# Kernel optimization log

Measured on AMD Instinct MI355X. Metric: run time of the kernel, lower is better.

Reference implementation:

```python
import jax, jax.numpy as jnp
import numpy as np
from jax import lax

K = 5          # CARAFE kernel_size
S = 2          # scale_factor (downsample stride)
GROUP = 1      # mask groups
ENC_PAD = 1    # (encoder_kernel-1)*dilation//2 with encoder_kernel=3


def _conv2d(x, w, b, stride, padding, dilation=1):
    y = lax.conv_general_dilated(
        x, w, window_strides=(stride, stride),
        padding=[(padding, padding), (padding, padding)],
        rhs_dilation=(dilation, dilation),
        dimension_numbers=('NCHW', 'OIHW', 'NCHW'))
    return y + b[None, :, None, None]


def setup_inputs() -> dict:
    key = jax.random.key(0)
    k1, k2, k3 = jax.random.split(key, 3)
    B, C, H, W = 4, 256, 128, 128
    COMP = 64
    x = jax.random.normal(k1, (B, C, H, W), dtype=jnp.float32)
    # xavier-uniform-ish scale for compressor, std=0.001 for content encoder (as in init_weights)
    w1 = jax.random.normal(k2, (COMP, C, 1, 1), dtype=jnp.float32) * (1.0 / np.sqrt(C))
    b1 = jnp.zeros((COMP,), dtype=jnp.float32)
    w2 = jax.random.normal(k3, (K * K * GROUP, COMP, 3, 3), dtype=jnp.float32) * 0.001
    b2 = jnp.zeros((K * K * GROUP,), dtype=jnp.float32)
    return {"x": x, "w1": w1, "b1": b1, "w2": w2, "b2": b2}


def _carafe_forward(x, w1, b1, w2, b2):
    B, C, H, W = x.shape
    compressed = _conv2d(x, w1, b1, stride=1, padding=0)           # (B, 64, H, W)
    mask = _conv2d(compressed, w2, b2, stride=S, padding=ENC_PAD)   # (B, K*K*G, Ho, Wo)
    Ho, Wo = mask.shape[2], mask.shape[3]
    # kernel_normalizer: softmax over the K*K window per group
    mask = jax.nn.softmax(mask.reshape(B, GROUP, K * K, Ho, Wo), axis=2)
    # feature_reassemble: fused unfold * mask sum — accumulate per kernel tap to
    # avoid materializing the full (B, C, K*K, Ho, Wo) tensor.
    pad = K // 2
    x_pad = jnp.pad(x, ((0, 0), (0, 0), (pad, pad), (pad, pad)))
    Cg = C // GROUP
    out = jnp.zeros((B, GROUP, Cg, Ho, Wo), dtype=x.dtype)
    for i in range(K):
        for j in range(K):
            patch = x_pad[:, :, i:i + S * (Ho - 1) + 1:S, j:j + S * (Wo - 1) + 1:S]
            patch = patch.reshape(B, GROUP, Cg, Ho, Wo)
            out = out + patch * mask[:, :, i * K + j][:, :, None]
    return out.reshape(B, C, Ho, Wo)


def reference(x, w1, b1, w2, b2):
    return _carafe_forward(x, w1, b1, w2, b2)
```

## Files before the change

### kernel.cpp

```cpp
#include <hip/hip_runtime.h>
#include <math.h>

#define BN   4
#define CN   256
#define HN   128
#define WN   128
#define COMP 64
#define KK   25
#define HO   64
#define WO   64

#define TB_OFF    36864
#define SM_OFF    37120
#define SM_SLICE  (BN * HO * KK * 64)
#define XT_OFF    (SM_OFF + SM_SLICE)
#define WS_NEED   ((size_t)(XT_OFF + (size_t)BN * HN * WN * CN / 2) * 4)

typedef short v8s  __attribute__((ext_vector_type(8)));
typedef float v16f __attribute__((ext_vector_type(16)));

__device__ inline ushort f2bf(float f) {
  unsigned u = __float_as_uint(f);
  return (ushort)((u + 0x7fffu + ((u >> 16) & 1u)) >> 16);
}

__global__ __launch_bounds__(256) void prep_kernel(
    const float* __restrict__ x, const float* __restrict__ w1,
    const float* __restrict__ b1, const float* __restrict__ w2,
    float* __restrict__ ws) {
  const int bid = blockIdx.x;
  const int tid = threadIdx.x;
  if (bid < 4096) {
    __shared__ float st[64][65];
    const int b = bid >> 10, h = (bid >> 3) & 127, bx = bid & 7;
    const int wt = bx & 1, ct = bx >> 1;
    const int w0 = wt * 64, c0 = ct * 64;
    {
      const int wl = tid & 63, cw = tid >> 6;
#pragma unroll
      for (int i = 0; i < 16; ++i) {
        int cl = cw * 16 + i;
        st[cl][wl] = x[((size_t)(b * CN + c0 + cl) * HN + h) * WN + w0 + wl];
      }
    }
    __syncthreads();
    ushort* xT = (ushort*)(ws + XT_OFF);
    const int cg = tid & 15, wl0 = tid >> 4;
#pragma unroll
    for (int wi = 0; wi < 4; ++wi) {
      int wl = wl0 + wi * 16;
      ushort4 o = make_ushort4(f2bf(st[cg * 4 + 0][wl]), f2bf(st[cg * 4 + 1][wl]),
                               f2bf(st[cg * 4 + 2][wl]), f2bf(st[cg * 4 + 3][wl]));
      *(ushort4*)(xT + ((size_t)((b * HN + h) * WN + w0 + wl)) * CN + c0 + cg * 4) = o;
    }
  } else {
    const int cid = bid - 4096;
    const int t = cid >> 2;
    const int chunk = (cid & 3) * 4 + (tid >> 6);
    const int lane = tid & 63;
    const int m = lane & 31, half = lane >> 5;
    const int c0 = chunk * 16 + half * 8;
    float acc[8] = {0.f, 0.f, 0.f, 0.f, 0.f, 0.f, 0.f, 0.f};
    if (m < KK) {
      for (int k = 0; k < COMP; ++k) {
        float wv = w2[(size_t)(m * COMP + k) * 9 + t];
        const float* w1r = w1 + (size_t)k * CN + c0;
        float4 a = *(const float4*)w1r;
        float4 bq = *(const float4*)(w1r + 4);
        acc[0] += wv * a.x;  acc[1] += wv * a.y;
        acc[2] += wv * a.z;  acc[3] += wv * a.w;
        acc[4] += wv * bq.x; acc[5] += wv * bq.y;
        acc[6] += wv * bq.z; acc[7] += wv * bq.w;
      }
    }
    ushort* wA = (ushort*)ws;
    ushort pk[8];
#pragma unroll
    for (int j = 0; j < 8; ++j) pk[j] = f2bf(acc[j]);
    *(ushort4*)(wA + ((size_t)(t * 16 + chunk) * 64 + lane) * 8) =
        make_ushort4(pk[0], pk[1], pk[2], pk[3]);
    *(ushort4*)(wA + ((size_t)(t * 16 + chunk) * 64 + lane) * 8 + 4) =
        make_ushort4(pk[4], pk[5], pk[6], pk[7]);
    if (chunk == 0 && lane < KK) {
      float tbv = 0.f;
      for (int k = 0; k < COMP; ++k)
        tbv += w2[(size_t)(lane * COMP + k) * 9 + t] * b1[k];
      ws[TB_OFF + lane * 9 + t] = tbv;
    }
  }
}

__global__ __launch_bounds__(512) void conv_softmax(
    const float* __restrict__ ws, const float* __restrict__ b2,
    float* __restrict__ sm) {
  const int ho = blockIdx.x, b = blockIdx.y;
  const int tid = threadIdx.x;
  const int lane = tid & 63;
  const int z = tid >> 6;
  const int n = lane & 31, half = lane >> 5;
  const ushort* xT = (const ushort*)(ws + XT_OFF);
  const ushort* wA = (const ushort*)ws;
  const int coff = z * 32 + half * 8;
  const v8s zero8 = {};
  v16f acc[2] = {{}, {}};

  __shared__ float red[8 * KK * 64];

#pragma unroll
  for (int dr = 0; dr < 3; ++dr) {
    const int r = 2 * ho + dr - 1;
    if (r < 0) continue;
#pragma unroll
    for (int dc = 0; dc < 3; ++dc) {
      const int t = dr * 3 + dc;
      const ushort* ap = wA + ((size_t)(t * 16 + z * 2) * 64 + lane) * 8;
      v8s af0 = *(const v8s*)ap;
      v8s af1 = *(const v8s*)(ap + 512);
      const size_t rowbase = (size_t)((b * HN + r) * WN);
#pragma unroll
      for (int wt = 0; wt < 2; ++wt) {
        const int wo = wt * 32 + n;
        const int q = 2 * wo + dc - 1;
        const bool bad = q < 0;
        const int qc = bad ? 0 : q;
        const ushort* bp = xT + (rowbase + qc) * CN + coff;
        v8s bf0 = *(const v8s*)bp;
        v8s bf1 = *(const v8s*)(bp + 16);
        if (dc == 0 && bad) { bf0 = zero8; bf1 = zero8; }
        acc[wt] = __builtin_amdgcn_mfma_f32_32x32x16_bf16(af0, bf0, acc[wt], 0, 0, 0);
        acc[wt] = __builtin_amdgcn_mfma_f32_32x32x16_bf16(af1, bf1, acc[wt], 0, 0, 0);
      }
    }
  }

#pragma unroll
  for (int wt = 0; wt < 2; ++wt) {
#pragma unroll
    for (int rg = 0; rg < 16; ++rg) {
      int m = (rg & 3) + 8 * (rg >> 2) + 4 * half;
      if (m < KK) red[(z * KK + m) * 64 + wt * 32 + n] = acc[wt][rg];
    }
  }
  __syncthreads();
  {
    const int wv = z, wo = lane;
    if (wv < 4) {
#pragma unroll
      for (int m = 0; m < KK; ++m)
        red[(wv * KK + m) * 64 + wo] += red[((wv + 4) * KK + m) * 64 + wo];
    }
    __syncthreads();
    if (wv < 2) {
#pragma unroll
      for (int m = 0; m < KK; ++m)
        red[(wv * KK + m) * 64 + wo] += red[((wv + 2) * KK + m) * 64 + wo];
    }
    __syncthreads();
  }
  if (tid < 64) {
    const int wo = tid;
    const float* tb = ws + TB_OFF;
    const float vr0 = (ho > 0) ? 1.f : 0.f;
    const float vq0 = (wo > 0) ? 1.f : 0.f;
    float logit[KK];
    float mx = -1e30f;
#pragma unroll
    for (int m = 0; m < KK; ++m) {
      const float* t9 = tb + m * 9;
      float l = b2[m]
              + vr0 * (vq0 * t9[0] + t9[1] + t9[2])
              +       (vq0 * t9[3] + t9[4] + t9[5])
              +       (vq0 * t9[6] + t9[7] + t9[8]);
      l += red[(0 * KK + m) * 64 + wo] + red[(1 * KK + m) * 64 + wo];
      logit[m] = l;
      mx = fmaxf(mx, l);
    }
    float ssum = 0.f;
#pragma unroll
    for (int m = 0; m < KK; ++m) {
      float e = __expf(logit[m] - mx);
      logit[m] = e;
      ssum += e;
    }
    float inv = 1.f / ssum;
    float* dst = sm + ((size_t)(b * HO + ho) * KK) * 64 + wo;
#pragma unroll
    for (int m = 0; m < KK; ++m) dst[(size_t)m * 64] = logit[m] * inv;
  }
}

__global__ __launch_bounds__(512) void gather_kernel(
    const float* __restrict__ x, const float* __restrict__ sm,
    float* __restrict__ out) {
  const int ho  = blockIdx.x;
  const int b   = blockIdx.y;
  const int z   = blockIdx.z;
  const int tid = threadIdx.x;
  const int wo  = tid & 63;
  const int wv  = tid >> 6;
  const int c_base = __builtin_amdgcn_readfirstlane(z * 64 + wv * 8);

  float smr[KK];
  {
    const float* smp = sm + ((size_t)(b * HO + ho) * KK) * 64 + wo;
#pragma unroll
    for (int m = 0; m < KK; ++m) smr[m] = smp[(size_t)m * 64];
  }

  const float* __restrict__ xb = x + (size_t)(b * CN) * (HN * WN);
  const int col = 2 * wo;
  const float wok = (wo > 0) ? 1.f : 0.f;
  const float w63 = (wo < 63) ? 1.f : 0.f;

  float2 g[2][5];
  auto load_g = [&](int ci, float2* dst) {
    const float* xc = xb + (size_t)(c_base + ci) * (HN * WN);
#pragma unroll
    for (int i = 0; i < 5; ++i) {
      int r = 2 * ho - 2 + i;
      dst[i] = (r >= 0 && r < HN) ? *(const float2*)(xc + r * WN + col)
                                  : make_float2(0.f, 0.f);
    }
  };
  load_g(0, g[0]);
  load_g(1, g[1]);

  for (int ci = 0; ci < 8; ++ci) {
    float2 v[5];
#pragma unroll
    for (int i = 0; i < 5; ++i) v[i] = g[ci & 1][i];
    if (ci + 2 < 8) load_g(ci + 2, g[ci & 1]);

    float acc2 = 0.f;
#pragma unroll
    for (int i = 0; i < 5; ++i) {
      float lx = wok * __shfl_up(v[i].x, 1, 64);
      float ly = wok * __shfl_up(v[i].y, 1, 64);
      float rx = w63 * __shfl_down(v[i].x, 1, 64);
      acc2 += lx * smr[i * 5 + 0] + ly * smr[i * 5 + 1]
            + v[i].x * smr[i * 5 + 2] + v[i].y * smr[i * 5 + 3]
            + rx * smr[i * 5 + 4];
    }
    out[(((size_t)(b * CN + c_base + ci)) * HO + ho) * WO + wo] = acc2;
  }
}

#define FB_WSTRIDE 240
#define FB_TB_OFF  (256 * FB_WSTRIDE)

__global__ __launch_bounds__(256) void compose_w_fb(
    const float* __restrict__ w1, const float* __restrict__ b1,
    const float* __restrict__ w2, float* __restrict__ ws) {
  int mt = blockIdx.x, c = threadIdx.x;
  float acc = 0.f;
#pragma unroll 8
  for (int k = 0; k < COMP; ++k)
    acc += w2[(size_t)(mt / 9 * COMP + k) * 9 + (mt % 9)] * w1[k * CN + c];
  ws[c * FB_WSTRIDE + mt] = acc;
  if (mt < FB_WSTRIDE - 225) ws[c * FB_WSTRIDE + 225 + mt] = 0.f;
  if (c == 0) {
    float tbv = 0.f;
    for (int k = 0; k < COMP; ++k)
      tbv += w2[(size_t)(mt / 9 * COMP + k) * 9 + (mt % 9)] * b1[k];
    ws[FB_TB_OFF + mt] = tbv;
  }
}

__global__ __launch_bounds__(1024, 4) void fused_fb(
    const float* __restrict__ x, const float* __restrict__ b2,
    const float* __restrict__ ws, float* __restrict__ out) {
  const int ho = blockIdx.x, b = blockIdx.y, tid = threadIdx.x;
  const int wo = tid & 63, wv = tid >> 6;
  const int c_base = __builtin_amdgcn_readfirstlane(wv * 16);
  const float* __restrict__ w2c = ws;
  const float* __restrict__ tb  = ws + FB_TB_OFF;
  __shared__ float red[8 * KK * 64];
  __shared__ float sm[KK * 64];
  const float* __restrict__ xb = x + (size_t)(b * CN) * (HN * WN);
  const int col = 2 * wo;
  float acc[KK];
#pragma unroll
  for (int m = 0; m < KK; ++m) acc[m] = 0.f;
  float2 xbuf[2][3];
  auto load_ch = [&](int ci, float2* dst) {
    const float* xc = xb + (size_t)(c_base + ci) * (HN * WN);
    dst[0] = (ho > 0) ? *(const float2*)(xc + (2 * ho - 1) * WN + col)
                      : make_float2(0.f, 0.f);
    dst[1] = *(const float2*)(xc + (2 * ho) * WN + col);
    dst[2] = *(const float2*)(xc + (2 * ho + 1) * WN + col);
  };
  load_ch(0, xbuf[0]);
  load_ch(1, xbuf[1]);
  const float wok = (wo > 0) ? 1.f : 0.f;
  for (int ci = 0; ci < 16; ++ci) {
    float2 r0 = xbuf[ci & 1][0], r1 = xbuf[ci & 1][1], r2 = xbuf[ci & 1][2];
    if (ci + 2 < 16) load_ch(ci + 2, xbuf[ci & 1]);
    float xv[9];
    xv[0] = wok * __shfl_up(r0.y, 1, 64); xv[1] = r0.x; xv[2] = r0.y;
    xv[3] = wok * __shfl_up(r1.y, 1, 64); xv[4] = r1.x; xv[5] = r1.y;
    xv[6] = wok * __shfl_up(r2.y, 1, 64); xv[7] = r2.x; xv[8] = r2.y;
    const float* __restrict__ wrow = w2c + (size_t)(c_base + ci) * FB_WSTRIDE;
#pragma unroll
    for (int m = 0; m < KK; ++m) {
      float a = acc[m];
#pragma unroll
      for (int t = 0; t < 9; ++t) a += wrow[m * 9 + t] * xv[t];
      acc[m] = a;
    }
  }
  float2 g[2][5];
  auto load_g = [&](int ci, float2* dst) {
    const float* xc = xb + (size_t)(c_base + ci) * (HN * WN);
#pragma unroll
    for (int i = 0; i < 5; ++i) {
      int r = 2 * ho - 2 + i;
      dst[i] = (r >= 0 && r < HN) ? *(const float2*)(xc + r * WN + col)
                                  : make_float2(0.f, 0.f);
    }
  };
  load_g(0, g[0]);
  load_g(1, g[1]);
  if (wv >= 8) {
#pragma unroll
    for (int m = 0; m < KK; ++m) red[((wv - 8) * KK + m) * 64 + wo] = acc[m];
  }
  __syncthreads();
  if (wv < 8) {
#pragma unroll
    for (int m = 0; m < KK; ++m) red[(wv * KK + m) * 64 + wo] += acc[m];
  }
  __syncthreads();
  if (wv < 4) {
#pragma unroll
    for (int m = 0; m < KK; ++m)
      red[(wv * KK + m) * 64 + wo] += red[((wv + 4) * KK + m) * 64 + wo];
  }
  __syncthreads();
  if (wv < 2) {
#pragma unroll
    for (int m = 0; m < KK; ++m)
      red[(wv * KK + m) * 64 + wo] += red[((wv + 2) * KK + m) * 64 + wo];
  }
  __syncthreads();
  if (tid < 64) {
    const float vr0 = (ho > 0) ? 1.f : 0.f;
    const float vq0 = (wo > 0) ? 1.f : 0.f;
    float logit[KK];
    float mx = -1e30f;
#pragma unroll
    for (int m = 0; m < KK; ++m) {
      const float* t9 = tb + m * 9;
      float l = b2[m]
              + vr0 * (vq0 * t9[0] + t9[1] + t9[2])
              +       (vq0 * t9[3] + t9[4] + t9[5])
              +       (vq0 * t9[6] + t9[7] + t9[8]);
      l += red[(0 * KK + m) * 64 + wo] + red[(1 * KK + m) * 64 + wo];
      logit[m] = l;
      mx = fmaxf(mx, l);
    }
    float s = 0.f;
#pragma unroll
    for (int m = 0; m < KK; ++m) {
      float e = __expf(logit[m] - mx);
      logit[m] = e;
      s += e;
    }
    float inv = 1.f / s;
#pragma unroll
    for (int m = 0; m < KK; ++m) sm[m * 64 + wo] = logit[m] * inv;
  }
  __syncthreads();
  float smr[KK];
#pragma unroll
  for (int m = 0; m < KK; ++m) smr[m] = sm[m * 64 + wo];
  const float w63 = (wo < 63) ? 1.f : 0.f;
  for (int ci = 0; ci < 16; ++ci) {
    float2 v[5];
#pragma unroll
    for (int i = 0; i < 5; ++i) v[i] = g[ci & 1][i];
    if (ci + 2 < 16) load_g(ci + 2, g[ci & 1]);
    float acc2 = 0.f;
#pragma unroll
    for (int i = 0; i < 5; ++i) {
      float lx = wok * __shfl_up(v[i].x, 1, 64);
      float ly = wok * __shfl_up(v[i].y, 1, 64);
      float rx = w63 * __shfl_down(v[i].x, 1, 64);
      acc2 += lx * smr[i * 5 + 0] + ly * smr[i * 5 + 1]
            + v[i].x * smr[i * 5 + 2] + v[i].y * smr[i * 5 + 3]
            + rx * smr[i * 5 + 4];
    }
    out[(((size_t)(b * CN + c_base + ci)) * HO + ho) * WO + wo] = acc2;
  }
}

extern "C" void kernel_launch(void* const* d_in, const int* in_sizes, int n_in,
                              void* d_out, int out_size, void* d_ws, size_t ws_size,
                              hipStream_t stream) {
  const float* x  = (const float*)d_in[0];
  const float* w1 = (const float*)d_in[1];
  const float* b1 = (const float*)d_in[2];
  const float* w2 = (const float*)d_in[3];
  const float* b2 = (const float*)d_in[4];
  float* out = (float*)d_out;
  float* ws  = (float*)d_ws;

  if (ws_size >= WS_NEED) {
    float* sm = ws + SM_OFF;
    hipLaunchKernelGGL(prep_kernel, dim3(4096 + 36), dim3(256), 0, stream,
                       x, w1, b1, w2, ws);
    hipLaunchKernelGGL(conv_softmax, dim3(HO, BN), dim3(512), 0, stream,
                       ws, b2, sm);
    hipLaunchKernelGGL(gather_kernel, dim3(HO, BN, 4), dim3(512), 0, stream,
                       x, sm, out);
  } else {
    hipLaunchKernelGGL(compose_w_fb, dim3(225), dim3(256), 0, stream,
                       w1, b1, w2, ws);
    hipLaunchKernelGGL(fused_fb, dim3(HO, BN), dim3(1024), 0, stream,
                       x, b2, ws, out);
  }
}
```

Measured before the change: 161.8 us.

## Fuse mask conv/softmax with gather into one 1024-thread kernel

Merges the conv_softmax and gather kernels into a single kernel per (ho, b) with 16 waves. Each wave handles one K-chunk of the MFMA mask conv and then gathers 16 channels. The softmax mask now passes through shared memory instead of a global buffer, and the x prefetch is issued before the reduction to hide its latency. This removes one launch and the global round trip of the mask. In exchange the grid shrinks to 256 blocks of 1024 threads, which may lower parallelism, and there is more shared-memory reduction work.

Measured after the change: 159.9 us. No clear change (-1.2%).

```diff
diff --git a/kernel.cpp b/kernel.cpp
--- a/kernel.cpp
+++ b/kernel.cpp
@@ -11,9 +11,7 @@
 #define WO   64
 
 #define TB_OFF    36864
-#define SM_OFF    37120
-#define SM_SLICE  (BN * HO * KK * 64)
-#define XT_OFF    (SM_OFF + SM_SLICE)
+#define XT_OFF    37120
 #define WS_NEED   ((size_t)(XT_OFF + (size_t)BN * HN * WN * CN / 2) * 4)
 
 typedef short v8s  __attribute__((ext_vector_type(8)));
@@ -90,21 +88,22 @@
   }
 }
 
-__global__ __launch_bounds__(512) void conv_softmax(
+__global__ __launch_bounds__(1024, 4) void conv_softmax_gather(
     const float* __restrict__ ws, const float* __restrict__ b2,
-    float* __restrict__ sm) {
+    const float* __restrict__ x, float* __restrict__ out) {
   const int ho = blockIdx.x, b = blockIdx.y;
   const int tid = threadIdx.x;
   const int lane = tid & 63;
-  const int z = tid >> 6;
+  const int wv = tid >> 6;
   const int n = lane & 31, half = lane >> 5;
   const ushort* xT = (const ushort*)(ws + XT_OFF);
   const ushort* wA = (const ushort*)ws;
-  const int coff = z * 32 + half * 8;
+  const int coff = wv * 16 + half * 8;
   const v8s zero8 = {};
   v16f acc[2] = {{}, {}};
 
   __shared__ float red[8 * KK * 64];
+  __shared__ float sml[KK * 64];
 
 #pragma unroll
   for (int dr = 0; dr < 3; ++dr) {
@@ -113,9 +112,8 @@
 #pragma unroll
     for (int dc = 0; dc < 3; ++dc) {
       const int t = dr * 3 + dc;
-      const ushort* ap = wA + ((size_t)(t * 16 + z * 2) * 64 + lane) * 8;
-      v8s af0 = *(const v8s*)ap;
-      v8s af1 = *(const v8s*)(ap + 512);
+      const ushort* ap = wA + ((size_t)(t * 16 + wv) * 64 + lane) * 8;
+      v8s af = *(const v8s*)ap;
       const size_t rowbase = (size_t)((b * HN + r) * WN);
 #pragma unroll
       for (int wt = 0; wt < 2; ++wt) {
@@ -124,41 +122,63 @@
         const bool bad = q < 0;
         const int qc = bad ? 0 : q;
         const ushort* bp = xT + (rowbase + qc) * CN + coff;
-        v8s bf0 = *(const v8s*)bp;
-        v8s bf1 = *(const v8s*)(bp + 16);
-        if (dc == 0 && bad) { bf0 = zero8; bf1 = zero8; }
-        acc[wt] = __builtin_amdgcn_mfma_f32_32x32x16_bf16(af0, bf0, acc[wt], 0, 0, 0);
-        acc[wt] = __builtin_amdgcn_mfma_f32_32x32x16_bf16(af1, bf1, acc[wt], 0, 0, 0);
+        v8s bf = *(const v8s*)bp;
+        if (dc == 0 && bad) bf = zero8;
+        acc[wt] = __builtin_amdgcn_mfma_f32_32x32x16_bf16(af, bf, acc[wt], 0, 0, 0);
       }
     }
   }
 
-#pragma unroll
-  for (int wt = 0; wt < 2; ++wt) {
-#pragma unroll
-    for (int rg = 0; rg < 16; ++rg) {
-      int m = (rg & 3) + 8 * (rg >> 2) + 4 * half;
-      if (m < KK) red[(z * KK + m) * 64 + wt * 32 + n] = acc[wt][rg];
-    }
-  }
-  __syncthreads();
-  {
-    const int wv = z, wo = lane;
-    if (wv < 4) {
-#pragma unroll
-      for (int m = 0; m < KK; ++m)
-        red[(wv * KK + m) * 64 + wo] += red[((wv + 4) * KK + m) * 64 + wo];
-    }
-    __syncthreads();
-    if (wv < 2) {
-#pragma unroll
-      for (int m = 0; m < KK; ++m)
-        red[(wv * KK + m) * 64 + wo] += red[((wv + 2) * KK + m) * 64 + wo];
-    }
-    __syncthreads();
-  }
+  const int wo = lane;
+  const int c_base = __builtin_amdgcn_readfirstlane(wv * 16);
+  const float* __restrict__ xb = x + (size_t)(b * CN) * (HN * WN);
+  const int col = 2 * wo;
+  float2 g[2][5];
+  auto load_g = [&](int ci, float2* dst) {
+    const float* xc = xb + (size_t)(c_base + ci) * (HN * WN);
+#pragma unroll
+    for (int i = 0; i < 5; ++i) {
+      int r = 2 * ho - 2 + i;
+      dst[i] = (r >= 0 && r < HN) ? *(const float2*)(xc + r * WN + col)
+                                  : make_float2(0.f, 0.f);
+    }
+  };
+  load_g(0, g[0]);
+  load_g(1, g[1]);
+
+  if (wv >= 8) {
+#pragma unroll
+    for (int wt = 0; wt < 2; ++wt)
+#pragma unroll
+      for (int rg = 0; rg < 16; ++rg) {
+        int m = (rg & 3) + 8 * (rg >> 2) + 4 * half;
+        if (m < KK) red[((wv - 8) * KK + m) * 64 + wt * 32 + n] = acc[wt][rg];
+      }
+  }
+  __syncthreads();
+  if (wv < 8) {
+#pragma unroll
+    for (int wt = 0; wt < 2; ++wt)
+#pragma unroll
+      for (int rg = 0; rg < 16; ++rg) {
+        int m = (rg & 3) + 8 * (rg >> 2) + 4 * half;
+        if (m < KK) red[(wv * KK + m) * 64 + wt * 32 + n] += acc[wt][rg];
+      }
+  }
+  __syncthreads();
+  if (wv < 4) {
+#pragma unroll
+    for (int m = 0; m < KK; ++m)
+      red[(wv * KK + m) * 64 + wo] += red[((wv + 4) * KK + m) * 64 + wo];
+  }
+  __syncthreads();
+  if (wv < 2) {
+#pragma unroll
+    for (int m = 0; m < KK; ++m)
+      red[(wv * KK + m) * 64 + wo] += red[((wv + 2) * KK + m) * 64 + wo];
+  }
+  __syncthreads();
   if (tid < 64) {
-    const int wo = tid;
     const float* tb = ws + TB_OFF;
     const float vr0 = (ho > 0) ? 1.f : 0.f;
     const float vq0 = (wo > 0) ? 1.f : 0.f;
@@ -183,53 +203,22 @@
       ssum += e;
     }
     float inv = 1.f / ssum;
-    float* dst = sm + ((size_t)(b * HO + ho) * KK) * 64 + wo;
-#pragma unroll
-    for (int m = 0; m < KK; ++m) dst[(size_t)m * 64] = logit[m] * inv;
-  }
-}
-
-__global__ __launch_bounds__(512) void gather_kernel(
-    const float* __restrict__ x, const float* __restrict__ sm,
-    float* __restrict__ out) {
-  const int ho  = blockIdx.x;
-  const int b   = blockIdx.y;
-  const int z   = blockIdx.z;
-  const int tid = threadIdx.x;
-  const int wo  = tid & 63;
-  const int wv  = tid >> 6;
-  const int c_base = __builtin_amdgcn_readfirstlane(z * 64 + wv * 8);
+#pragma unroll
+    for (int m = 0; m < KK; ++m) sml[m * 64 + wo] = logit[m] * inv;
+  }
+  __syncthreads();
 
   float smr[KK];
-  {
-    const float* smp = sm + ((size_t)(b * HO + ho) * KK) * 64 + wo;
-#pragma unroll
-    for (int m = 0; m < KK; ++m) smr[m] = smp[(size_t)m * 64];
-  }
-
-  const float* __restrict__ xb = x + (size_t)(b * CN) * (HN * WN);
-  const int col = 2 * wo;
+#pragma unroll
+  for (int m = 0; m < KK; ++m) smr[m] = sml[m * 64 + wo];
+
   const float wok = (wo > 0) ? 1.f : 0.f;
   const float w63 = (wo < 63) ? 1.f : 0.f;
-
-  float2 g[2][5];
-  auto load_g = [&](int ci, float2* dst) {
-    const float* xc = xb + (size_t)(c_base + ci) * (HN * WN);
-#pragma unroll
-    for (int i = 0; i < 5; ++i) {
-      int r = 2 * ho - 2 + i;
-      dst[i] = (r >= 0 && r < HN) ? *(const float2*)(xc + r * WN + col)
-                                  : make_float2(0.f, 0.f);
-    }
-  };
-  load_g(0, g[0]);
-  load_g(1, g[1]);
-
-  for (int ci = 0; ci < 8; ++ci) {
+  for (int ci = 0; ci < 16; ++ci) {
     float2 v[5];
 #pragma unroll
     for (int i = 0; i < 5; ++i) v[i] = g[ci & 1][i];
-    if (ci + 2 < 8) load_g(ci + 2, g[ci & 1]);
+    if (ci + 2 < 16) load_g(ci + 2, g[ci & 1]);
 
     float acc2 = 0.f;
 #pragma unroll
@@ -405,13 +394,10 @@
   float* ws  = (float*)d_ws;
 
   if (ws_size >= WS_NEED) {
-    float* sm = ws + SM_OFF;
     hipLaunchKernelGGL(prep_kernel, dim3(4096 + 36), dim3(256), 0, stream,
                        x, w1, b1, w2, ws);
-    hipLaunchKernelGGL(conv_softmax, dim3(HO, BN), dim3(512), 0, stream,
-                       ws, b2, sm);
-    hipLaunchKernelGGL(gather_kernel, dim3(HO, BN, 4), dim3(512), 0, stream,
-                       x, sm, out);
+    hipLaunchKernelGGL(conv_softmax_gather, dim3(HO, BN), dim3(1024), 0, stream,
+                       ws, b2, x, out);
   } else {
     hipLaunchKernelGGL(compose_w_fb, dim3(225), dim3(256), 0, stream,
                        w1, b1, w2, ws);
```
